# Performance work log

Measured on AMD Instinct MI355X. Metric: run time of the kernel, lower is better.

## Reference

```python
import jax, jax.numpy as jnp
import numpy as np
from jax import lax


def _lstm_layer(x, W_ih, W_hh, b_ih, b_hh):
    """Single LSTM layer, batch_first x: [B, T, in] -> (out [B,T,H], h_n [B,H], c_n [B,H]).
    PyTorch gate order: i, f, g, o."""
    B, T, _ = x.shape
    H = W_hh.shape[1]
    # Precompute input contributions for all timesteps (one big GEMM).
    xg = jnp.einsum('bti,gi->btg', x, W_ih) + b_ih + b_hh  # [B, T, 4H]
    h0 = jnp.zeros((B, H), dtype=x.dtype)
    c0 = jnp.zeros((B, H), dtype=x.dtype)

    def step(carry, g_t):
        h, c = carry
        gates = g_t + h @ W_hh.T  # [B, 4H]
        i, f, g, o = jnp.split(gates, 4, axis=-1)
        i = jax.nn.sigmoid(i)
        f = jax.nn.sigmoid(f)
        g = jnp.tanh(g)
        o = jax.nn.sigmoid(o)
        c = f * c + i * g
        h = o * jnp.tanh(c)
        return (h, c), h

    (h_n, c_n), hs = lax.scan(step, (h0, c0), jnp.swapaxes(xg, 0, 1))  # hs: [T, B, H]
    return jnp.swapaxes(hs, 0, 1), h_n, c_n


def setup_inputs() -> dict:
    key = jax.random.key(0)
    ks = jax.random.split(key, 12)
    H = 128
    IN = 1
    B, T = 256, 2048
    s = 1.0 / np.sqrt(H)  # PyTorch default init scale

    def u(k, shape):
        return jax.random.uniform(k, shape, jnp.float32, -s, s)

    return {
        'x': jax.random.normal(ks[0], (B, T, IN), jnp.float32),
        'W_ih_l0': u(ks[1], (4 * H, IN)),
        'W_hh_l0': u(ks[2], (4 * H, H)),
        'b_ih_l0': u(ks[3], (4 * H,)),
        'b_hh_l0': u(ks[4], (4 * H,)),
        'W_ih_l1': u(ks[5], (4 * H, H)),
        'W_hh_l1': u(ks[6], (4 * H, H)),
        'b_ih_l1': u(ks[7], (4 * H,)),
        'b_hh_l1': u(ks[8], (4 * H,)),
        'W_fc': u(ks[9], (1, H)),
        'b_fc': u(ks[10], (1,)),
    }


def reference(x, W_ih_l0, W_hh_l0, b_ih_l0, b_hh_l0,
              W_ih_l1, W_hh_l1, b_ih_l1, b_hh_l1, W_fc, b_fc):
    out0, h0, c0 = _lstm_layer(x, W_ih_l0, W_hh_l0, b_ih_l0, b_hh_l0)
    out1, h1, c1 = _lstm_layer(out0, W_ih_l1, W_hh_l1, b_ih_l1, b_hh_l1)
    last = out1[:, -1, :]                 # [B, H]
    y = last @ W_fc.T + b_fc              # [B, 1]
    h_n = jnp.stack([h0, h1], axis=0)     # [num_layers, B, H]
    c_n = jnp.stack([c0, c1], axis=0)
    return (y, h_n, c_n)
```

## Files before the change

### kernel.cpp

```cpp
#include <hip/hip_runtime.h>

#define T_SEQ 2048
#define HDIM  128
#define GDIM  512
#define BATCH 256

typedef _Float16 f16;
typedef _Float16 f16x2 __attribute__((ext_vector_type(2)));
typedef _Float16 f16x8 __attribute__((ext_vector_type(8)));

#if __has_builtin(__builtin_amdgcn_fdot2)
__device__ __forceinline__ float dot2(f16x2 a, f16x2 b, float c) {
    return __builtin_amdgcn_fdot2(a, b, c, false);
}
#else
__device__ __forceinline__ float dot2(f16x2 a, f16x2 b, float c) {
    return c + (float)a[0] * (float)b[0] + (float)a[1] * (float)b[1];
}
#endif

__device__ __forceinline__ f16x2 mk2(float a, float b) {
    f16x2 r; r[0] = (f16)a; r[1] = (f16)b; return r;
}
__device__ __forceinline__ f16x2 pr(f16x8 v, int m) {
    f16x2 r; r[0] = v[2 * m]; r[1] = v[2 * m + 1]; return r;
}

__device__ __forceinline__ float sigm(float x) {
    return __builtin_amdgcn_rcpf(1.0f + __expf(-x));
}
__device__ __forceinline__ float tanh_fast(float x) {
    float e = __expf(2.0f * x);
    return 1.0f - 2.0f * __builtin_amdgcn_rcpf(e + 1.0f);
}

__global__ __launch_bounds__(512, 2)
void lstm_fused(const float* __restrict__ x,
                const float* __restrict__ Wih0,
                const float* __restrict__ Whh0,
                const float* __restrict__ bih0,
                const float* __restrict__ bhh0,
                const float* __restrict__ Wih1,
                const float* __restrict__ Whh1,
                const float* __restrict__ bih1,
                const float* __restrict__ bhh1,
                const float* __restrict__ Wfc,
                const float* __restrict__ bfc,
                float* __restrict__ out)
{
    __shared__ __align__(16) f16   wh1s[GDIM * 72];
    __shared__ __align__(16) float xs[T_SEQ];
    __shared__ __align__(16) f16   h0h[HDIM];
    __shared__ __align__(16) f16   h1h[HDIM];
    __shared__ float h0f[HDIM], h1f[HDIM];
    __shared__ float g0[GDIM], g1[GDIM];

    const int t = threadIdx.x;
    const int b = blockIdx.x;

    ((float4*)xs)[t] = ((const float4*)(x + (size_t)b * T_SEQ))[t];

    f16x2 w0[64];
    f16x2 wi[64];
    f16x2 wl[32];
    {
        const float4* p0 = (const float4*)(Whh0 + t * HDIM);
        const float4* p1 = (const float4*)(Wih1 + t * HDIM);
        const float4* p2 = (const float4*)(Whh1 + t * HDIM);
#pragma unroll
        for (int c = 0; c < 32; ++c) {
            float4 v = p0[c];
            w0[2 * c]     = mk2(v.x, v.y);
            w0[2 * c + 1] = mk2(v.z, v.w);
        }
#pragma unroll
        for (int c = 0; c < 32; ++c) {
            float4 v = p1[c];
            wi[2 * c]     = mk2(v.x, v.y);
            wi[2 * c + 1] = mk2(v.z, v.w);
        }
#pragma unroll
        for (int c = 0; c < 16; ++c) {
            float4 v = p2[c];
            wl[2 * c]     = mk2(v.x, v.y);
            wl[2 * c + 1] = mk2(v.z, v.w);
        }
        f16x2* dst = (f16x2*)(wh1s + t * 72);
#pragma unroll
        for (int c = 0; c < 16; ++c) {
            float4 v = p2[16 + c];
            dst[2 * c]     = mk2(v.x, v.y);
            dst[2 * c + 1] = mk2(v.z, v.w);
        }
    }
    const float wx0   = Wih0[t];
    const float bias0 = bih0[t] + bhh0[t];
    const float bias1 = bih1[t] + bhh1[t];

    if (t < HDIM) {
        h0h[t] = (f16)0.f; h1h[t] = (f16)0.f;
        h0f[t] = 0.f;      h1f[t] = 0.f;
    }
    float c0r = 0.f, c1r = 0.f;
    __syncthreads();

    const f16x8* h0p  = (const f16x8*)h0h;
    const f16x8* h1p  = (const f16x8*)h1h;
    const f16x8* wrow = (const f16x8*)(wh1s + t * 72);

    for (int i = 0; i <= T_SEQ; ++i) {
        float a0 = (i < T_SEQ ? xs[i] : 0.f) * wx0 + bias0;
        float a1 = bias1;
#pragma unroll
        for (int c = 0; c < 16; ++c) {
            f16x8 h = h0p[c];
#pragma unroll
            for (int m = 0; m < 4; ++m) {
                f16x2 hp = pr(h, m);
                a0 = dot2(w0[4 * c + m], hp, a0);
                a1 = dot2(wi[4 * c + m], hp, a1);
            }
        }
#pragma unroll
        for (int c = 0; c < 8; ++c) {
            f16x8 h = h1p[c];
#pragma unroll
            for (int m = 0; m < 4; ++m)
                a1 = dot2(wl[4 * c + m], pr(h, m), a1);
        }
#pragma unroll
        for (int c = 0; c < 8; ++c) {
            f16x8 h = h1p[8 + c];
            f16x8 w = wrow[c];
#pragma unroll
            for (int m = 0; m < 4; ++m)
                a1 = dot2(pr(w, m), pr(h, m), a1);
        }
        g0[t] = a0;
        g1[t] = a1;
        __syncthreads();

        if (t < 128) {
            if (i < T_SEQ) {
                float gi = sigm(g0[t]);
                float gf = sigm(g0[t + 128]);
                float gg = tanh_fast(g0[t + 256]);
                float go = sigm(g0[t + 384]);
                c0r = gf * c0r + gi * gg;
                float h = go * tanh_fast(c0r);
                h0h[t] = (f16)h;
                h0f[t] = h;
            }
        } else if (t < 256) {
            if (i >= 1) {
                int j = t - 128;
                float gi = sigm(g1[j]);
                float gf = sigm(g1[j + 128]);
                float gg = tanh_fast(g1[j + 256]);
                float go = sigm(g1[j + 384]);
                c1r = gf * c1r + gi * gg;
                float h = go * tanh_fast(c1r);
                h1h[j] = (f16)h;
                h1f[j] = h;
            }
        }
        __syncthreads();
    }

    float* hn = out + BATCH;
    float* cn = out + BATCH + 2 * BATCH * HDIM;
    if (t < 128) {
        hn[(size_t)b * HDIM + t] = h0f[t];
        cn[(size_t)b * HDIM + t] = c0r;
    } else if (t < 256) {
        int j = t - 128;
        hn[BATCH * HDIM + (size_t)b * HDIM + j] = h1f[j];
        cn[BATCH * HDIM + (size_t)b * HDIM + j] = c1r;
    }
    if (t < 64) {
        float p = h1f[t] * Wfc[t] + h1f[t + 64] * Wfc[t + 64];
#pragma unroll
        for (int o = 32; o >= 1; o >>= 1) p += __shfl_down(p, o);
        if (t == 0) out[b] = p + bfc[0];
    }
}

extern "C" void kernel_launch(void* const* d_in, const int* in_sizes, int n_in,
                              void* d_out, int out_size, void* d_ws, size_t ws_size,
                              hipStream_t stream) {
    const float* x    = (const float*)d_in[0];
    const float* Wih0 = (const float*)d_in[1];
    const float* Whh0 = (const float*)d_in[2];
    const float* bih0 = (const float*)d_in[3];
    const float* bhh0 = (const float*)d_in[4];
    const float* Wih1 = (const float*)d_in[5];
    const float* Whh1 = (const float*)d_in[6];
    const float* bih1 = (const float*)d_in[7];
    const float* bhh1 = (const float*)d_in[8];
    const float* Wfc  = (const float*)d_in[9];
    const float* bfc  = (const float*)d_in[10];
    lstm_fused<<<BATCH, 512, 0, stream>>>(x, Wih0, Whh0, bih0, bhh0,
                                          Wih1, Whh1, bih1, bhh1,
                                          Wfc, bfc, (float*)d_out);
}
```

Before: 2.653 ms.

## Interleave gate rows per thread, exchange gates via shuffles, double-buffer hidden state

Each thread now owns row gate*128+u, so the four gates of one hidden unit sit in adjacent lanes and are gathered with warp shuffles rather than through shared memory. This removes one of the two __syncthreads per timestep, and double-buffering h0/h1 makes the remaining barrier enough. All of W_hh1 now lives in registers instead of half of it in LDS, with launch bounds relaxed to 1 block per CU so more VGPRs are available. Split accumulators add ILP, but the heavier register footprint and redundant activation math in every lane may hurt occupancy.

```diff
diff --git a/kernel.cpp b/kernel.cpp
--- a/kernel.cpp
+++ b/kernel.cpp
@@ -34,7 +34,7 @@
     return 1.0f - 2.0f * __builtin_amdgcn_rcpf(e + 1.0f);
 }
 
-__global__ __launch_bounds__(512, 2)
+__global__ __launch_bounds__(512, 1)
 void lstm_fused(const float* __restrict__ x,
                 const float* __restrict__ Wih0,
                 const float* __restrict__ Whh0,
@@ -48,140 +48,121 @@
                 const float* __restrict__ bfc,
                 float* __restrict__ out)
 {
-    __shared__ __align__(16) f16   wh1s[GDIM * 72];
     __shared__ __align__(16) float xs[T_SEQ];
-    __shared__ __align__(16) f16   h0h[HDIM];
-    __shared__ __align__(16) f16   h1h[HDIM];
-    __shared__ float h0f[HDIM], h1f[HDIM];
-    __shared__ float g0[GDIM], g1[GDIM];
+    __shared__ __align__(16) f16   h0b[2][HDIM];
+    __shared__ __align__(16) f16   h1b[2][HDIM];
+    __shared__ float ysum[8];
 
-    const int t = threadIdx.x;
-    const int b = blockIdx.x;
+    const int t    = threadIdx.x;
+    const int b    = blockIdx.x;
+    const int gate = t & 3;
+    const int u    = t >> 2;
+    const int row  = gate * HDIM + u;
 
     ((float4*)xs)[t] = ((const float4*)(x + (size_t)b * T_SEQ))[t];
 
     f16x2 w0[64];
     f16x2 wi[64];
-    f16x2 wl[32];
+    f16x2 wl[64];
     {
-        const float4* p0 = (const float4*)(Whh0 + t * HDIM);
-        const float4* p1 = (const float4*)(Wih1 + t * HDIM);
-        const float4* p2 = (const float4*)(Whh1 + t * HDIM);
+        const float4* p0 = (const float4*)(Whh0 + (size_t)row * HDIM);
+        const float4* p1 = (const float4*)(Wih1 + (size_t)row * HDIM);
+        const float4* p2 = (const float4*)(Whh1 + (size_t)row * HDIM);
 #pragma unroll
         for (int c = 0; c < 32; ++c) {
             float4 v = p0[c];
-            w0[2 * c]     = mk2(v.x, v.y);
-            w0[2 * c + 1] = mk2(v.z, v.w);
+            w0[2 * c] = mk2(v.x, v.y); w0[2 * c + 1] = mk2(v.z, v.w);
         }
 #pragma unroll
         for (int c = 0; c < 32; ++c) {
             float4 v = p1[c];
-            wi[2 * c]     = mk2(v.x, v.y);
-            wi[2 * c + 1] = mk2(v.z, v.w);
+            wi[2 * c] = mk2(v.x, v.y); wi[2 * c + 1] = mk2(v.z, v.w);
         }
 #pragma unroll
-        for (int c = 0; c < 16; ++c) {
+        for (int c = 0; c < 32; ++c) {
             float4 v = p2[c];
-            wl[2 * c]     = mk2(v.x, v.y);
-            wl[2 * c + 1] = mk2(v.z, v.w);
-        }
-        f16x2* dst = (f16x2*)(wh1s + t * 72);
-#pragma unroll
-        for (int c = 0; c < 16; ++c) {
-            float4 v = p2[16 + c];
-            dst[2 * c]     = mk2(v.x, v.y);
-            dst[2 * c + 1] = mk2(v.z, v.w);
+            wl[2 * c] = mk2(v.x, v.y); wl[2 * c + 1] = mk2(v.z, v.w);
         }
     }
-    const float wx0   = Wih0[t];
-    const float bias0 = bih0[t] + bhh0[t];
-    const float bias1 = bih1[t] + bhh1[t];
+    const float wx0   = Wih0[row];
+    const float bias0 = bih0[row] + bhh0[row];
+    const float bias1 = bih1[row] + bhh1[row];
 
-    if (t < HDIM) {
-        h0h[t] = (f16)0.f; h1h[t] = (f16)0.f;
-        h0f[t] = 0.f;      h1f[t] = 0.f;
-    }
+    if (t < HDIM) { h0b[0][t] = (f16)0.f; h1b[0][t] = (f16)0.f; }
     float c0r = 0.f, c1r = 0.f;
+    float h0fin = 0.f, h1fin = 0.f;
     __syncthreads();
 
-    const f16x8* h0p  = (const f16x8*)h0h;
-    const f16x8* h1p  = (const f16x8*)h1h;
-    const f16x8* wrow = (const f16x8*)(wh1s + t * 72);
+    const int lb = (t & 63) & ~3;
 
     for (int i = 0; i <= T_SEQ; ++i) {
-        float a0 = (i < T_SEQ ? xs[i] : 0.f) * wx0 + bias0;
-        float a1 = bias1;
+        const int p = i & 1, q = p ^ 1;
+        const f16x8* h0p = (const f16x8*)h0b[p];
+        const f16x8* h1p = (const f16x8*)h1b[p];
+
+        float a0a = (i < T_SEQ ? xs[i] : 0.f) * wx0 + bias0, a0b = 0.f;
+        float a1a = bias1, a1b = 0.f;
 #pragma unroll
-        for (int c = 0; c < 16; ++c) {
-            f16x8 h = h0p[c];
+        for (int c = 0; c < 16; c += 2) {
+            f16x8 ha = h0p[c], hb = h0p[c + 1];
 #pragma unroll
             for (int m = 0; m < 4; ++m) {
-                f16x2 hp = pr(h, m);
-                a0 = dot2(w0[4 * c + m], hp, a0);
-                a1 = dot2(wi[4 * c + m], hp, a1);
+                a0a = dot2(w0[4 * c + m],     pr(ha, m), a0a);
+                a1a = dot2(wi[4 * c + m],     pr(ha, m), a1a);
+                a0b = dot2(w0[4 * c + 4 + m], pr(hb, m), a0b);
+                a1b = dot2(wi[4 * c + 4 + m], pr(hb, m), a1b);
             }
         }
 #pragma unroll
-        for (int c = 0; c < 8; ++c) {
-            f16x8 h = h1p[c];
+        for (int c = 0; c < 16; c += 2) {
+            f16x8 ha = h1p[c], hb = h1p[c + 1];
 #pragma unroll
-            for (int m = 0; m < 4; ++m)
-                a1 = dot2(wl[4 * c + m], pr(h, m), a1);
+            for (int m = 0; m < 4; ++m) {
+                a1a = dot2(wl[4 * c + m],     pr(ha, m), a1a);
+                a1b = dot2(wl[4 * c + 4 + m], pr(hb, m), a1b);
+            }
         }
-#pragma unroll
-        for (int c = 0; c < 8; ++c) {
-            f16x8 h = h1p[8 + c];
-            f16x8 w = wrow[c];
-#pragma unroll
-            for (int m = 0; m < 4; ++m)
-                a1 = dot2(pr(w, m), pr(h, m), a1);
+        const float a0 = a0a + a0b;
+        const float a1 = a1a + a1b;
+
+        float gi0 = __shfl(a0, lb + 0), gf0 = __shfl(a0, lb + 1);
+        float gg0 = __shfl(a0, lb + 2), go0 = __shfl(a0, lb + 3);
+        float gi1 = __shfl(a1, lb + 0), gf1 = __shfl(a1, lb + 1);
+        float gg1 = __shfl(a1, lb + 2), go1 = __shfl(a1, lb + 3);
+
+        if (i < T_SEQ) {
+            c0r   = sigm(gf0) * c0r + sigm(gi0) * tanh_fast(gg0);
+            h0fin = sigm(go0) * tanh_fast(c0r);
+            if (gate == 0) h0b[q][u] = (f16)h0fin;
         }
-        g0[t] = a0;
-        g1[t] = a1;
-        __syncthreads();
-
-        if (t < 128) {
-            if (i < T_SEQ) {
-                float gi = sigm(g0[t]);
-                float gf = sigm(g0[t + 128]);
-                float gg = tanh_fast(g0[t + 256]);
-                float go = sigm(g0[t + 384]);
-                c0r = gf * c0r + gi * gg;
-                float h = go * tanh_fast(c0r);
-                h0h[t] = (f16)h;
-                h0f[t] = h;
-            }
-        } else if (t < 256) {
-            if (i >= 1) {
-                int j = t - 128;
-                float gi = sigm(g1[j]);
-                float gf = sigm(g1[j + 128]);
-                float gg = tanh_fast(g1[j + 256]);
-                float go = sigm(g1[j + 384]);
-                c1r = gf * c1r + gi * gg;
-                float h = go * tanh_fast(c1r);
-                h1h[j] = (f16)h;
-                h1f[j] = h;
-            }
+        if (i >= 1) {
+            c1r   = sigm(gf1) * c1r + sigm(gi1) * tanh_fast(gg1);
+            h1fin = sigm(go1) * tanh_fast(c1r);
+            if (gate == 0) h1b[q][u] = (f16)h1fin;
+        } else if (gate == 0) {
+            h1b[q][u] = (f16)0.f;
         }
         __syncthreads();
     }
 
     float* hn = out + BATCH;
     float* cn = out + BATCH + 2 * BATCH * HDIM;
-    if (t < 128) {
-        hn[(size_t)b * HDIM + t] = h0f[t];
-        cn[(size_t)b * HDIM + t] = c0r;
-    } else if (t < 256) {
-        int j = t - 128;
-        hn[BATCH * HDIM + (size_t)b * HDIM + j] = h1f[j];
-        cn[BATCH * HDIM + (size_t)b * HDIM + j] = c1r;
+    if (gate == 0) {
+        hn[(size_t)b * HDIM + u] = h0fin;
+        cn[(size_t)b * HDIM + u] = c0r;
+        hn[BATCH * HDIM + (size_t)b * HDIM + u] = h1fin;
+        cn[BATCH * HDIM + (size_t)b * HDIM + u] = c1r;
     }
-    if (t < 64) {
-        float p = h1f[t] * Wfc[t] + h1f[t + 64] * Wfc[t + 64];
+    float part = (gate == 0) ? h1fin * Wfc[u] : 0.f;
 #pragma unroll
-        for (int o = 32; o >= 1; o >>= 1) p += __shfl_down(p, o);
-        if (t == 0) out[b] = p + bfc[0];
+    for (int o = 32; o >= 1; o >>= 1) part += __shfl_xor(part, o);
+    if ((t & 63) == 0) ysum[t >> 6] = part;
+    __syncthreads();
+    if (t == 0) {
+        float s = 0.f;
+#pragma unroll
+        for (int w = 0; w < 8; ++w) s += ysum[w];
+        out[b] = s + bfc[0];
     }
 }
 
```

After: 2.809 ms. +5.9%, slower.
